# Optimization experiments

Hardware: AMD Instinct MI355X
Metric: run time of the kernel (lower is better)

## Reference

```python
import jax, jax.numpy as jnp
import numpy as np

N_AGENTS, OBS_DIM, HID, ACT_DIM = 8192, 64, 128, 16


def setup_inputs() -> dict:
    key = jax.random.key(0)
    k = jax.random.split(key, 8)
    obs_agents = jax.random.normal(k[0], (N_AGENTS, OBS_DIM), dtype=jnp.float32)
    # binary adjacency, {0,1}, int32 (index/mask semantics, non-differentiable)
    adj = jax.random.randint(k[1], (N_AGENTS, N_AGENTS), 0, 2, dtype=jnp.int32)
    def lin(kk, fan_in, fan_out):
        lim = 1.0 / np.sqrt(fan_in)
        kw, kb = jax.random.split(kk)
        W = jax.random.uniform(kw, (fan_in, fan_out), jnp.float32, -lim, lim)
        b = jax.random.uniform(kb, (fan_out,), jnp.float32, -lim, lim)
        return W, b
    W1, b1 = lin(k[2], OBS_DIM, HID)          # encoder
    W2, b2 = lin(k[3], 2 * HID, HID)          # actor layer 1
    W3, b3 = lin(k[4], HID, ACT_DIM)          # actor layer 2
    return {"obs_agents": obs_agents, "adj": adj,
            "W1": W1, "b1": b1, "W2": W2, "b2": b2, "W3": W3, "b3": b3}


def reference(obs_agents, adj, W1, b1, W2, b2, W3, b3):
    # per-agent encode: h = tanh(obs @ W1 + b1)  -> [N, HID]
    h = jnp.tanh(obs_agents @ W1 + b1)
    # neighbor mean message: mean of h[j] over j with adj[i,j]!=0, zeros if no neighbors
    a = adj.astype(h.dtype)                      # [N, N] binary
    deg = jnp.sum(a, axis=1, keepdims=True)      # [N, 1]
    msg = (a @ h) / jnp.maximum(deg, 1.0)        # zero rows stay zero
    # actor MLP on concat([h, msg])
    combined = jnp.concatenate([h, msg], axis=-1)            # [N, 2*HID]
    hid = jnp.tanh(combined @ W2 + b2)                        # [N, HID]
    logits = hid @ W3 + b3                                    # [N, ACT_DIM]
    return logits
```

## Files before the change

### kernel.cpp

```cpp
#include <hip/hip_runtime.h>
#include <stdint.h>
#include <math.h>

#define NAG 8192
#define NC  128
#define NSPLIT 16
#define LDB2 136

typedef __attribute__((ext_vector_type(8))) short short8;
typedef __attribute__((ext_vector_type(4))) float floatx4;

__device__ __forceinline__ float bf2f(unsigned short u) {
    union { uint32_t i; float f; } v; v.i = ((uint32_t)u) << 16; return v.f;
}
__device__ __forceinline__ unsigned short f2bf(float f) {
    union { float f; uint32_t i; } v; v.f = f;
    uint32_t x = v.i;
    return (unsigned short)((x + 0x7FFFu + ((x >> 16) & 1u)) >> 16);
}
__device__ __forceinline__ unsigned short f2h(float f) {
    union { _Float16 h; unsigned short u; } v; v.h = (_Float16)f; return v.u;
}
__device__ __forceinline__ float h2f(unsigned short u) {
    union { _Float16 h; unsigned short u; } v; v.u = u; return (float)v.h;
}
__device__ __forceinline__ bool detect_f32(const void* W1, int t) {
    const unsigned short* w = (const unsigned short*)W1;
    int l = t & 63, big = 0;
    #pragma unroll
    for (int j = 0; j < 8; ++j) {
        float v = bf2f(w[l * 8 + j]);
        if (!(fabsf(v) <= 1e6f)) big = 1;
    }
    return __ballot(big) != 0ull;
}

__global__ __launch_bounds__(256) void kA_pack_encode(
    const int* __restrict__ adj,
    unsigned long long* __restrict__ bits,
    const void* __restrict__ obs,
    const void* __restrict__ W1,
    const void* __restrict__ b1,
    float* __restrict__ h_f32,
    unsigned short* __restrict__ hT)
{
    const int t = threadIdx.x;
    if (blockIdx.x < 2048) {
        const int lane = t & 63;
        const int gw = blockIdx.x * 4 + (t >> 6);
        for (int it = 0; it < 32; ++it) {
            size_t u = ((size_t)it * 8192 + gw) * 4;
            size_t col = u * 64 + lane;
            unsigned long long m0 = __ballot(adj[col]       != 0);
            unsigned long long m1 = __ballot(adj[col + 64]  != 0);
            unsigned long long m2 = __ballot(adj[col + 128] != 0);
            unsigned long long m3 = __ballot(adj[col + 192] != 0);
            if (lane == 0) {
                bits[u]     = m0;
                bits[u + 1] = m1;
                bits[u + 2] = m2;
                bits[u + 3] = m3;
            }
        }
        return;
    }
    __shared__ float obs_lds[32][68];
    __shared__ unsigned short ht_lds[128][33];
    const int abase = (blockIdx.x - 2048) * 32;
    const bool isf = detect_f32(W1, t);

    {
        int a = t >> 3, c0 = (t & 7) * 8;
        if (isf) {
            const float* p = (const float*)obs;
            #pragma unroll
            for (int j = 0; j < 8; ++j)
                obs_lds[a][c0 + j] = p[(size_t)(abase + a) * 64 + c0 + j];
        } else {
            const unsigned short* p = (const unsigned short*)obs;
            #pragma unroll
            for (int j = 0; j < 8; ++j)
                obs_lds[a][c0 + j] = bf2f(p[(size_t)(abase + a) * 64 + c0 + j]);
        }
    }
    __syncthreads();

    const int o = t & 127;
    const int half = t >> 7;
    float acc[16];
    if (isf) {
        const float* Wp = (const float*)W1;
        float bias = ((const float*)b1)[o];
        #pragma unroll
        for (int i = 0; i < 16; ++i) acc[i] = bias;
        for (int k0 = 0; k0 < 64; k0 += 8) {
            float w[8];
            #pragma unroll
            for (int j = 0; j < 8; ++j) w[j] = Wp[(k0 + j) * 128 + o];
            #pragma unroll
            for (int j = 0; j < 8; ++j)
                #pragma unroll
                for (int i = 0; i < 16; ++i)
                    acc[i] = fmaf(obs_lds[half * 16 + i][k0 + j], w[j], acc[i]);
        }
    } else {
        const unsigned short* Wp = (const unsigned short*)W1;
        float bias = bf2f(((const unsigned short*)b1)[o]);
        #pragma unroll
        for (int i = 0; i < 16; ++i) acc[i] = bias;
        for (int k0 = 0; k0 < 64; k0 += 8) {
            float w[8];
            #pragma unroll
            for (int j = 0; j < 8; ++j) w[j] = bf2f(Wp[(k0 + j) * 128 + o]);
            #pragma unroll
            for (int j = 0; j < 8; ++j)
                #pragma unroll
                for (int i = 0; i < 16; ++i)
                    acc[i] = fmaf(obs_lds[half * 16 + i][k0 + j], w[j], acc[i]);
        }
    }
    #pragma unroll
    for (int i = 0; i < 16; ++i) {
        float th = tanhf(acc[i]);
        int a = half * 16 + i;
        h_f32[(size_t)(abase + a) * 128 + o] = th;
        ht_lds[o][a] = f2bf(th);
    }
    __syncthreads();

    for (int p = 0; p < 16; ++p) {
        int n = p * 8 + (t >> 5);
        int a = t & 31;
        hT[(size_t)n * NAG + abase + a] = ht_lds[n][a];
    }
}

__global__ __launch_bounds__(256, 4) void k2_msggemm(
    const uint32_t* __restrict__ bits,
    const unsigned short* __restrict__ hT,
    unsigned short* __restrict__ Cp16)
{
    __shared__ __align__(16) unsigned short Blds[128 * LDB2];
    const int t = threadIdx.x;
    const int mtile = blockIdx.x & 63;
    const int ks = blockIdx.x >> 6;
    const int row0 = mtile * 128;
    const int kbeg = ks * 512;

    const int wave = t >> 6, lane = t & 63;
    const int fm = lane & 15, quad = lane >> 4;

    floatx4 acc0[8], acc1[8];
    #pragma unroll
    for (int i = 0; i < 8; ++i) { acc0[i] = (floatx4)0.f; acc1[i] = (floatx4)0.f; }

    const int arow0 = row0 + wave * 32 + fm;
    const uint32_t* aWp0 = bits + (size_t)arow0 * 256 + (kbeg >> 5);
    const uint32_t* aWp1 = aWp0 + 16 * 256;

    for (int ss = 0; ss < 4; ++ss) {
        if (ss) __syncthreads();
        #pragma unroll
        for (int i = 0; i < 8; ++i) {
            int idx = i * 256 + t;
            int row = idx >> 4, ch = idx & 15;
            uint4 v = *reinterpret_cast<const uint4*>(hT + (size_t)row * NAG + kbeg + ss * 128 + ch * 8);
            *reinterpret_cast<uint4*>(&Blds[row * LDB2 + ch * 8]) = v;
        }
        int4 a0 = *reinterpret_cast<const int4*>(aWp0 + ss * 4);
        int4 a1 = *reinterpret_cast<const int4*>(aWp1 + ss * 4);
        uint32_t aw0[4] = {(uint32_t)a0.x, (uint32_t)a0.y, (uint32_t)a0.z, (uint32_t)a0.w};
        uint32_t aw1[4] = {(uint32_t)a1.x, (uint32_t)a1.y, (uint32_t)a1.z, (uint32_t)a1.w};
        __syncthreads();
        #pragma unroll
        for (int kw = 0; kw < 4; ++kw) {
            uint32_t b0 = (aw0[kw] >> (quad * 8)) & 0xFFu;
            uint32_t b1 = (aw1[kw] >> (quad * 8)) & 0xFFu;
            union { uint32_t u[4]; short8 s; } af0, af1;
            #pragma unroll
            for (int p = 0; p < 4; ++p) {
                uint32_t bb0 = b0 >> (2 * p);
                uint32_t bb1 = b1 >> (2 * p);
                af0.u[p] = ((bb0 & 1u) | ((bb0 & 2u) << 15)) * 0x3F80u;
                af1.u[p] = ((bb1 & 1u) | ((bb1 & 2u) << 15)) * 0x3F80u;
            }
            #pragma unroll
            for (int j = 0; j < 8; ++j) {
                short8 bf = *reinterpret_cast<const short8*>(&Blds[(j * 16 + fm) * LDB2 + kw * 32 + quad * 8]);
                acc0[j] = __builtin_amdgcn_mfma_f32_16x16x32_bf16(af0.s, bf, acc0[j], 0, 0, 0);
                acc1[j] = __builtin_amdgcn_mfma_f32_16x16x32_bf16(af1.s, bf, acc1[j], 0, 0, 0);
            }
        }
    }

    unsigned short* out = Cp16 + (size_t)ks * (NAG * NC);
    #pragma unroll
    for (int j = 0; j < 8; ++j) {
        int col = j * 16 + fm;
        #pragma unroll
        for (int r = 0; r < 4; ++r) {
            int row = row0 + wave * 32 + quad * 4 + r;
            out[(size_t)row * NC + col]        = f2h(acc0[j][r]);
            out[(size_t)(row + 16) * NC + col] = f2h(acc1[j][r]);
        }
    }
}

__global__ __launch_bounds__(256) void k3_actor(
    const float* __restrict__ h_f32,
    const unsigned short* __restrict__ Cp16,
    const unsigned long long* __restrict__ bits,
    const void* __restrict__ W1,
    const void* __restrict__ W2,
    const void* __restrict__ b2,
    const void* __restrict__ W3,
    const void* __restrict__ b3,
    void* __restrict__ out)
{
    __shared__ float4 comb4[8][66];
    __shared__ float hid[8][132];
    __shared__ int degp[8][33];
    __shared__ float inv_lds[8];
    const int t = threadIdx.x;
    const int abase = blockIdx.x * 8;
    const bool isf = detect_f32(W1, t);
    const size_t PS = (size_t)NAG * NC;

    {
        int a = t >> 5, j = t & 31;
        const unsigned long long* bp = bits + (size_t)(abase + a) * 128 + j * 4;
        degp[a][j] = __popcll(bp[0]) + __popcll(bp[1]) + __popcll(bp[2]) + __popcll(bp[3]);
    }
    __syncthreads();
    if (t < 8) {
        int d = 0;
        #pragma unroll
        for (int j = 0; j < 32; ++j) d += degp[t][j];
        inv_lds[t] = 1.0f / fmaxf((float)d, 1.0f);
    }
    __syncthreads();

    #pragma unroll
    for (int jj = 0; jj < 2; ++jj) {
        int idx = jj * 256 + t;
        int a = idx >> 6, q = idx & 63;
        float4 v;
        if (q < 32) {
            v = *reinterpret_cast<const float4*>(h_f32 + (size_t)(abase + a) * 128 + q * 4);
        } else {
            int f = (q - 32) * 4;
            float s0 = 0.f, s1 = 0.f, s2 = 0.f, s3 = 0.f;
            #pragma unroll
            for (int s = 0; s < NSPLIT; ++s) {
                ushort4 p = *reinterpret_cast<const ushort4*>(Cp16 + s * PS + (size_t)(abase + a) * NC + f);
                s0 += h2f(p.x); s1 += h2f(p.y); s2 += h2f(p.z); s3 += h2f(p.w);
            }
            float sc = inv_lds[a];
            v = make_float4(s0 * sc, s1 * sc, s2 * sc, s3 * sc);
        }
        comb4[a][q] = v;
    }
    __syncthreads();

    const int o = t & 127, half = t >> 7;
    float acc[4];
    if (isf) {
        const float* Wp = (const float*)W2;
        float bias = ((const float*)b2)[o];
        #pragma unroll
        for (int i = 0; i < 4; ++i) acc[i] = bias;
        for (int cq = 0; cq < 64; ++cq) {
            float w0 = Wp[(cq * 4 + 0) * 128 + o];
            float w1 = Wp[(cq * 4 + 1) * 128 + o];
            float w2 = Wp[(cq * 4 + 2) * 128 + o];
            float w3 = Wp[(cq * 4 + 3) * 128 + o];
            #pragma unroll
            for (int i = 0; i < 4; ++i) {
                float4 v = comb4[half * 4 + i][cq];
                acc[i] = fmaf(v.x, w0, acc[i]);
                acc[i] = fmaf(v.y, w1, acc[i]);
                acc[i] = fmaf(v.z, w2, acc[i]);
                acc[i] = fmaf(v.w, w3, acc[i]);
            }
        }
    } else {
        const unsigned short* Wp = (const unsigned short*)W2;
        float bias = bf2f(((const unsigned short*)b2)[o]);
        #pragma unroll
        for (int i = 0; i < 4; ++i) acc[i] = bias;
        for (int cq = 0; cq < 64; ++cq) {
            float w0 = bf2f(Wp[(cq * 4 + 0) * 128 + o]);
            float w1 = bf2f(Wp[(cq * 4 + 1) * 128 + o]);
            float w2 = bf2f(Wp[(cq * 4 + 2) * 128 + o]);
            float w3 = bf2f(Wp[(cq * 4 + 3) * 128 + o]);
            #pragma unroll
            for (int i = 0; i < 4; ++i) {
                float4 v = comb4[half * 4 + i][cq];
                acc[i] = fmaf(v.x, w0, acc[i]);
                acc[i] = fmaf(v.y, w1, acc[i]);
                acc[i] = fmaf(v.z, w2, acc[i]);
                acc[i] = fmaf(v.w, w3, acc[i]);
            }
        }
    }
    #pragma unroll
    for (int i = 0; i < 4; ++i)
        hid[half * 4 + i][o] = tanhf(acc[i]);
    __syncthreads();

    if (t < 128) {
        const int q = t & 15, ar = t >> 4;
        float l;
        if (isf) {
            const float* Wp = (const float*)W3;
            l = ((const float*)b3)[q];
            #pragma unroll 4
            for (int oo = 0; oo < 128; ++oo)
                l = fmaf(hid[ar][oo], Wp[oo * 16 + q], l);
        } else {
            const unsigned short* Wp = (const unsigned short*)W3;
            l = bf2f(((const unsigned short*)b3)[q]);
            #pragma unroll 4
            for (int oo = 0; oo < 128; ++oo)
                l = fmaf(hid[ar][oo], bf2f(Wp[oo * 16 + q]), l);
        }
        size_t i0 = (size_t)(abase + ar) * 16 + q;
        if (isf) ((float*)out)[i0] = l;
        else     ((unsigned short*)out)[i0] = f2bf(l);
    }
}

extern "C" void kernel_launch(void* const* d_in, const int* in_sizes, int n_in,
                              void* d_out, int out_size, void* d_ws, size_t ws_size,
                              hipStream_t stream) {
    const void* obs = d_in[0];
    const int*  adj = (const int*)d_in[1];
    const void* W1  = d_in[2];
    const void* b1  = d_in[3];
    const void* W2  = d_in[4];
    const void* b2  = d_in[5];
    const void* W3  = d_in[6];
    const void* b3  = d_in[7];

    char* ws = (char*)d_ws;
    unsigned short* hT   = (unsigned short*)(ws);
    float*          h_f32= (float*)(ws + 2097152);
    unsigned short* Cp16 = (unsigned short*)(ws + 6291456);
    unsigned long long* bits = (unsigned long long*)(ws + 39845888);

    hipLaunchKernelGGL(kA_pack_encode, dim3(2304), dim3(256), 0, stream,
                       adj, bits, obs, W1, b1, h_f32, hT);
    hipLaunchKernelGGL(k2_msggemm, dim3(1024), dim3(256), 0, stream,
                       (const uint32_t*)bits, hT, Cp16);
    hipLaunchKernelGGL(k3_actor, dim3(1024), dim3(256), 0, stream,
                       h_f32, Cp16, bits, W1, W2, b2, W3, b3, d_out);
}
```

Baseline: 451.0 us.

## Pre-tile hT with LDS padding and stage it via direct global-to-LDS loads

The encoder now writes the transposed hidden matrix into contiguous 128x136 padded tiles, so each k-chunk the message GEMM needs is one contiguous block. The GEMM then fills LDS with 16-byte global_load_lds copies instead of loading through registers and storing to LDS. The aim is to cut VGPR traffic and LDS store instructions in the staging path and make the loads fully contiguous. It costs slightly more workspace for padding, and it relies on the builtin's lane-addressing and synchronisation semantics being handled correctly.

```diff
diff --git a/kernel.cpp b/kernel.cpp
--- a/kernel.cpp
+++ b/kernel.cpp
@@ -6,6 +6,7 @@
 #define NC  128
 #define NSPLIT 16
 #define LDB2 136
+#define TILE_SH (128 * LDB2)
 
 typedef __attribute__((ext_vector_type(8))) short short8;
 typedef __attribute__((ext_vector_type(4))) float floatx4;
@@ -23,6 +24,12 @@
 }
 __device__ __forceinline__ float h2f(unsigned short u) {
     union { _Float16 h; unsigned short u; } v; v.u = u; return (float)v.h;
+}
+__device__ __forceinline__ void gld_lds16(const void* g, void* l) {
+    __builtin_amdgcn_global_load_lds(
+        (__attribute__((address_space(1))) void*)g,
+        (__attribute__((address_space(3))) void*)l,
+        16, 0, 0);
 }
 __device__ __forceinline__ bool detect_f32(const void* W1, int t) {
     const unsigned short* w = (const unsigned short*)W1;
@@ -42,7 +49,7 @@
     const void* __restrict__ W1,
     const void* __restrict__ b1,
     float* __restrict__ h_f32,
-    unsigned short* __restrict__ hT)
+    unsigned short* __restrict__ hT2)
 {
     const int t = threadIdx.x;
     if (blockIdx.x < 2048) {
@@ -128,24 +135,24 @@
     }
     __syncthreads();
 
+    unsigned short* htile = hT2 + (size_t)(abase >> 7) * TILE_SH + (abase & 127);
     for (int p = 0; p < 16; ++p) {
         int n = p * 8 + (t >> 5);
         int a = t & 31;
-        hT[(size_t)n * NAG + abase + a] = ht_lds[n][a];
+        htile[n * LDB2 + a] = ht_lds[n][a];
     }
 }
 
 __global__ __launch_bounds__(256, 4) void k2_msggemm(
     const uint32_t* __restrict__ bits,
-    const unsigned short* __restrict__ hT,
+    const unsigned short* __restrict__ hT2,
     unsigned short* __restrict__ Cp16)
 {
-    __shared__ __align__(16) unsigned short Blds[128 * LDB2];
+    __shared__ __align__(16) unsigned short Blds[TILE_SH];
     const int t = threadIdx.x;
     const int mtile = blockIdx.x & 63;
     const int ks = blockIdx.x >> 6;
     const int row0 = mtile * 128;
-    const int kbeg = ks * 512;
 
     const int wave = t >> 6, lane = t & 63;
     const int fm = lane & 15, quad = lane >> 4;
@@ -155,17 +162,20 @@
     for (int i = 0; i < 8; ++i) { acc0[i] = (floatx4)0.f; acc1[i] = (floatx4)0.f; }
 
     const int arow0 = row0 + wave * 32 + fm;
-    const uint32_t* aWp0 = bits + (size_t)arow0 * 256 + (kbeg >> 5);
+    const uint32_t* aWp0 = bits + (size_t)arow0 * 256 + ks * 16;
     const uint32_t* aWp1 = aWp0 + 16 * 256;
 
+    #pragma unroll 1
     for (int ss = 0; ss < 4; ++ss) {
         if (ss) __syncthreads();
-        #pragma unroll
-        for (int i = 0; i < 8; ++i) {
-            int idx = i * 256 + t;
-            int row = idx >> 4, ch = idx & 15;
-            uint4 v = *reinterpret_cast<const uint4*>(hT + (size_t)row * NAG + kbeg + ss * 128 + ch * 8);
-            *reinterpret_cast<uint4*>(&Blds[row * LDB2 + ch * 8]) = v;
+        {
+            const char* src = (const char*)(hT2 + (size_t)(ks * 4 + ss) * TILE_SH) + lane * 16;
+            char* dst = (char*)&Blds[0];
+            #pragma unroll
+            for (int i = 0; i < 9; ++i) {
+                int c = wave + i * 4;
+                if (c < 34) gld_lds16(src + c * 1024, dst + c * 1024);
+            }
         }
         int4 a0 = *reinterpret_cast<const int4*>(aWp0 + ss * 4);
         int4 a1 = *reinterpret_cast<const int4*>(aWp1 + ss * 4);
@@ -343,15 +353,15 @@
     const void* b3  = d_in[7];
 
     char* ws = (char*)d_ws;
-    unsigned short* hT   = (unsigned short*)(ws);
-    float*          h_f32= (float*)(ws + 2097152);
-    unsigned short* Cp16 = (unsigned short*)(ws + 6291456);
-    unsigned long long* bits = (unsigned long long*)(ws + 39845888);
+    unsigned short* hT2  = (unsigned short*)(ws);
+    float*          h_f32= (float*)(ws + 2228224);
+    unsigned short* Cp16 = (unsigned short*)(ws + 6422528);
+    unsigned long long* bits = (unsigned long long*)(ws + 39976960);
 
     hipLaunchKernelGGL(kA_pack_encode, dim3(2304), dim3(256), 0, stream,
-                       adj, bits, obs, W1, b1, h_f32, hT);
+                       adj, bits, obs, W1, b1, h_f32, hT2);
     hipLaunchKernelGGL(k2_msggemm, dim3(1024), dim3(256), 0, stream,
-                       (const uint32_t*)bits, hT, Cp16);
+                       (const uint32_t*)bits, hT2, Cp16);
     hipLaunchKernelGGL(k3_actor, dim3(1024), dim3(256), 0, stream,
                        h_f32, Cp16, bits, W1, W2, b2, W3, b3, d_out);
 }
```

Measured after the change: 437.9 us. 1.03x faster.
